# Kernel optimization log

Measured on AMD Instinct MI355X. Metric: run time of the kernel, lower is better.

## Reference

```python
import jax, jax.numpy as jnp
import numpy as np

A = -0.75  # torch bicubic coefficient
K = 5
K2 = K * K
IN_CH = 32 * 2 + 169 + 16 * 2 + 1  # 266
TIMESTEP = 0.5


def _cubic_w(t):
    # t in [0,1); weights for taps at offsets -1,0,1,2 (torch cubic convolution, A=-0.75)
    w1 = ((A + 2.0) * t - (A + 3.0)) * t * t + 1.0
    s = 1.0 - t
    w2 = ((A + 2.0) * s - (A + 3.0)) * s * s + 1.0
    u = t + 1.0
    w0 = ((A * u - 5.0 * A) * u + 8.0 * A) * u - 4.0 * A
    v = 2.0 - t
    w3 = ((A * v - 5.0 * A) * v + 8.0 * A) * v - 4.0 * A
    return (w0, w1, w2, w3)


def _conv3(x, w, b):
    y = jax.lax.conv_general_dilated(x, w, (1, 1), 'SAME',
                                     dimension_numbers=('NCHW', 'OIHW', 'NCHW'))
    return y + b[None, :, None, None]


def _lrelu(x):
    return jnp.where(x >= 0, x, 0.1 * x)


def _kernel_pred(x, w1, b1, w2, b2, w3, b3, ow, ob, ww, wb):
    f = _lrelu(_conv3(x, w1, b1))
    f = _lrelu(_conv3(f, w2, b2))
    f = _lrelu(_conv3(f, w3, b3))
    offsets = _conv3(f, ow, ob)                      # (B, 2*K2, H, W)
    weights = jax.nn.softmax(_conv3(f, ww, wb), axis=1)  # (B, K2, H, W)
    return offsets, weights


def _adacof_sample(image, offsets, weights):
    # bicubic grid_sample(padding_mode='border', align_corners=True) + weighted combine
    b, c, h, w = image.shape
    k2 = weights.shape[1]
    gx = jnp.arange(w, dtype=image.dtype)
    gy = jnp.arange(h, dtype=image.dtype)
    dx = offsets[:, 0::2]                # (b,k2,h,w)
    dy = offsets[:, 1::2]
    # with align_corners=True, normalize->unnormalize is identity
    sx = gx[None, None, None, :] + dx
    sy = gy[None, None, :, None] + dy
    x0 = jnp.floor(sx); tx = sx - x0
    y0 = jnp.floor(sy); ty = sy - y0
    wx = _cubic_w(tx)
    wy = _cubic_w(ty)
    xi = [jnp.clip(x0 + (i - 1.0), 0, w - 1).astype(jnp.int32) for i in range(4)]
    yi = [jnp.clip(y0 + (i - 1.0), 0, h - 1).astype(jnp.int32) for i in range(4)]
    imgf = image.reshape(b, c, h * w)
    gather = jax.vmap(lambda im, idx: im[:, idx])   # (c,hw),(n,)->(c,n)
    acc = jnp.zeros((b, c, k2, h, w), image.dtype)
    for i in range(4):
        for j in range(4):
            idx = (yi[i] * w + xi[j]).reshape(b, -1)
            g = gather(imgf, idx).reshape(b, c, k2, h, w)
            acc = acc + g * (wy[i] * wx[j])[:, None]
    return jnp.einsum('bckhw,bkhw->bchw', acc, weights)


def setup_inputs() -> dict:
    key = jax.random.key(0)
    ks = iter(jax.random.split(key, 64))
    d = {}
    d['frame1'] = jax.random.normal(next(ks), (2, 3, 256, 256), jnp.float32)
    d['frame2'] = jax.random.normal(next(ks), (2, 3, 256, 256), jnp.float32)
    d['feat1'] = jax.random.normal(next(ks), (2, 32, 256, 256), jnp.float32)
    d['feat2'] = jax.random.normal(next(ks), (2, 32, 256, 256), jnp.float32)
    d['corr'] = jax.random.normal(next(ks), (2, 169, 256, 256), jnp.float32)

    def conv_w(o, i):
        return jax.random.normal(next(ks), (o, i, 3, 3), jnp.float32) * 0.05

    # full-res encoder
    d['fr_w1'] = conv_w(16, 3); d['fr_b1'] = jnp.zeros((16,), jnp.float32)
    d['fr_w2'] = conv_w(16, 16); d['fr_b2'] = jnp.zeros((16,), jnp.float32)
    # default grid offsets for offset_head bias (dx,dy interleaved)
    off_bias = []
    for i in range(K):
        for j in range(K):
            off_bias.extend([j - K // 2, i - K // 2])
    off_bias = jnp.asarray(off_bias, jnp.float32)
    for p in ('kp1', 'kp2'):
        d[p + '_w1'] = conv_w(256, IN_CH); d[p + '_b1'] = jnp.zeros((256,), jnp.float32)
        d[p + '_w2'] = conv_w(256, 256); d[p + '_b2'] = jnp.zeros((256,), jnp.float32)
        d[p + '_w3'] = conv_w(128, 256); d[p + '_b3'] = jnp.zeros((128,), jnp.float32)
        d[p + '_ow'] = jax.random.normal(next(ks), (2 * K2, 128, 3, 3), jnp.float32) * 0.01
        d[p + '_ob'] = off_bias
        d[p + '_ww'] = jax.random.normal(next(ks), (K2, 128, 3, 3), jnp.float32) * 0.01
        d[p + '_wb'] = jnp.full((K2,), 1.0 / K2, jnp.float32)
    d['bl_w1'] = conv_w(64, IN_CH); d['bl_b1'] = jnp.zeros((64,), jnp.float32)
    d['bl_w2'] = conv_w(1, 64); d['bl_b2'] = jnp.zeros((1,), jnp.float32)
    return d


def reference(frame1, frame2, feat1, feat2, corr,
              fr_w1, fr_b1, fr_w2, fr_b2,
              kp1_w1, kp1_b1, kp1_w2, kp1_b2, kp1_w3, kp1_b3, kp1_ow, kp1_ob, kp1_ww, kp1_wb,
              kp2_w1, kp2_b1, kp2_w2, kp2_b2, kp2_w3, kp2_b3, kp2_ow, kp2_ob, kp2_ww, kp2_wb,
              bl_w1, bl_b1, bl_w2, bl_b2):
    b, _, h, w = frame1.shape
    fr1 = _lrelu(_conv3(_lrelu(_conv3(frame1, fr_w1, fr_b1)), fr_w2, fr_b2))
    fr2 = _lrelu(_conv3(_lrelu(_conv3(frame2, fr_w1, fr_b1)), fr_w2, fr_b2))
    t_map = jnp.full((b, 1, h, w), TIMESTEP, frame1.dtype)
    combined = jnp.concatenate([feat1, feat2, corr, fr1, fr2, t_map], axis=1)
    offsets1, weights1 = _kernel_pred(combined, kp1_w1, kp1_b1, kp1_w2, kp1_b2,
                                      kp1_w3, kp1_b3, kp1_ow, kp1_ob, kp1_ww, kp1_wb)
    offsets2, weights2 = _kernel_pred(combined, kp2_w1, kp2_b1, kp2_w2, kp2_b2,
                                      kp2_w3, kp2_b3, kp2_ow, kp2_ob, kp2_ww, kp2_wb)
    sample1 = _adacof_sample(frame1, offsets1, weights1)
    sample2 = _adacof_sample(frame2, offsets2, weights2)
    blend = jax.nn.sigmoid(_conv3(_lrelu(_conv3(combined, bl_w1, bl_b1)), bl_w2, bl_b2))
    output = blend * sample1 + (1.0 - blend) * sample2
    return (output, blend, offsets1, offsets2, weights1, weights2)
```

## Files before the change

kernel.cpp:

```cpp
#include <hip/hip_runtime.h>
#include <cstdint>
#include <cstddef>

#define H 256
#define W 256
#define HW (H*W)
#define BATCH 2
#define CIN_TILE 4

typedef __bf16 bf16x8 __attribute__((ext_vector_type(8)));
typedef float f32x4 __attribute__((ext_vector_type(4)));
typedef __attribute__((address_space(1))) uint32_t gu32_t;
typedef __attribute__((address_space(3))) uint32_t lu32_t;

__device__ __forceinline__ void async16(const void* g, void* l) {
  __builtin_amdgcn_global_load_lds((const gu32_t*)g, (lu32_t*)l, 16, 0, 0);
}

__device__ __forceinline__ ushort f2bf(float f) {
  uint u = __float_as_uint(f);
  return (ushort)((u + 0x7FFFu + ((u >> 16) & 1u)) >> 16);
}
__device__ __forceinline__ float lrelu_f(float v) { return v >= 0.f ? v : 0.1f * v; }

template<int EPI>
__global__ __launch_bounds__(256) void convmm_k(
    const ushort* __restrict__ act, const ushort* __restrict__ wgt,
    const float* __restrict__ bias, ushort* __restrict__ dstb,
    float* __restrict__ dsto, float* __restrict__ dstw,
    const ushort* __restrict__ zpage, int Cin, int CoutS)
{
  __shared__ __align__(16) ushort s_w[2304 * 8];
  __shared__ __align__(16) ushort s_b[1536 * 8];

  const int tid = threadIdx.x;
  const int sp = blockIdx.x;
  const int bx = (sp & 7) * 32, by = (sp >> 3) * 8;
  const int co0 = blockIdx.y * 64;
  const int wv = tid >> 6, lane = tid & 63;
  const int c = lane & 15, kq = lane >> 4;
  const int oy = wv * 2;

  int wsrc[9];
#pragma unroll
  for (int it = 0; it < 9; ++it) {
    int i = tid + it * 256;
    int co = i & 63, tk = i >> 6, tap = tk >> 2, kg = tk & 3;
    wsrc[it] = ((co0 + co) * 9 + tap) * Cin + kg * 8;
  }
  int bsrc[6];
#pragma unroll
  for (int it = 0; it < 6; ++it) {
    int i = tid + it * 256;
    int kg = i / 384, px = i - kg * 384;
    int row = px / 34, xx = px - row * 34;
    int gy = by + row - 1, gx = bx + xx - 1;
    bool ok = (px < 340) && ((unsigned)gy < (unsigned)H) && ((unsigned)gx < (unsigned)W);
    bsrc[it] = ok ? ((gy * W + gx) * Cin + kg * 8) : -1;
  }

  f32x4 acc[4][4];
#pragma unroll
  for (int a = 0; a < 4; ++a)
#pragma unroll
    for (int b2 = 0; b2 < 4; ++b2) acc[a][b2] = (f32x4){0.f, 0.f, 0.f, 0.f};

  const int nch = Cin >> 5;
  for (int ch = 0; ch < nch; ++ch) {
    const int c0 = ch << 5;
    __syncthreads();
#pragma unroll
    for (int it = 0; it < 9; ++it)
      async16(wgt + wsrc[it] + c0, &s_w[(size_t)(tid + it * 256) * 8]);
#pragma unroll
    for (int it = 0; it < 6; ++it) {
      const ushort* g = (bsrc[it] < 0) ? zpage : (act + bsrc[it] + c0);
      async16(g, &s_b[(size_t)(tid + it * 256) * 8]);
    }
    __syncthreads();

#pragma unroll
    for (int t = 0; t < 9; ++t) {
      const int dy = t / 3 - 1, dx = t % 3 - 1;
      bf16x8 B[4];
#pragma unroll
      for (int pf = 0; pf < 4; ++pf) {
        int p = (oy + (pf >> 1) + dy + 1) * 34 + (pf & 1) * 16 + dx + 1 + c;
        B[pf] = *(const bf16x8*)&s_b[(size_t)(kq * 384 + p) * 8];
      }
#pragma unroll
      for (int cf = 0; cf < 4; ++cf) {
        bf16x8 A = *(const bf16x8*)&s_w[(size_t)((t * 4 + kq) * 64 + cf * 16 + c) * 8];
#pragma unroll
        for (int pf = 0; pf < 4; ++pf)
          acc[cf][pf] = __builtin_amdgcn_mfma_f32_16x16x32_bf16(A, B[pf], acc[cf][pf], 0, 0, 0);
      }
    }
  }

  const int r4 = kq * 4;
#pragma unroll
  for (int cf = 0; cf < 4; ++cf) {
    int cob = co0 + cf * 16 + r4;
#pragma unroll
    for (int pf = 0; pf < 4; ++pf) {
      int gx2 = bx + (pf & 1) * 16 + c;
      int gy2 = by + oy + (pf >> 1);
      int gpix = gy2 * W + gx2;
      f32x4 v = acc[cf][pf];
      const float4 bv = *(const float4*)&bias[cob];
      if constexpr (EPI == 0) {
        ushort4 ov;
        float f0 = lrelu_f(v[0] + bv.x);
        float f1 = lrelu_f(v[1] + bv.y);
        float f2 = lrelu_f(v[2] + bv.z);
        float f3 = lrelu_f(v[3] + bv.w);
        ov.x = f2bf(f0); ov.y = f2bf(f1); ov.z = f2bf(f2); ov.w = f2bf(f3);
        *(ushort4*)&dstb[(size_t)gpix * CoutS + cob] = ov;
      } else {
        const float* bvp = &bv.x;
#pragma unroll
        for (int r = 0; r < 4; ++r) {
          int coa = cob + r;
          if (coa < 75) {
            float f = v[r] + bvp[r];
            if (coa < 50) dsto[(size_t)coa * HW + gpix] = f;
            else          dstw[(size_t)(coa - 50) * HW + gpix] = f;
          }
        }
      }
    }
  }
}

template<int CIN>
__global__ __launch_bounds__(256) void conv_fr_k(
    const float* __restrict__ sA, const float* __restrict__ sB, int mode,
    const float* __restrict__ wgt, const float* __restrict__ bias,
    float* __restrict__ dst)
{
  const int z = blockIdx.y;
  const float* src = (mode == 0)
      ? (((z >> 1) ? sB : sA) + (size_t)(z & 1) * 3 * HW)
      : (sA + (size_t)z * 16 * HW);
  float* out = dst + (size_t)z * 16 * HW;

  const int sp = blockIdx.x;
  const int bx = (sp & 7) * 32, by = (sp >> 3) * 32;
  const int tid = threadIdx.x;
  const int tx = tid & 15, ty = tid >> 4;

  __shared__ float s_in[CIN_TILE][34][36];
  float acc[16][2][2];
#pragma unroll
  for (int co = 0; co < 16; ++co) {
    acc[co][0][0] = 0.f; acc[co][0][1] = 0.f;
    acc[co][1][0] = 0.f; acc[co][1][1] = 0.f;
  }

  for (int c0 = 0; c0 < CIN; c0 += CIN_TILE) {
    __syncthreads();
    const int nst = CIN_TILE * 34 * 34;
    for (int i = tid; i < nst; i += 256) {
      int ci = i / (34 * 34);
      int r = i - ci * (34 * 34);
      int yy = r / 34;
      int xx = r - yy * 34;
      int gy = by + yy - 1, gx = bx + xx - 1;
      int cc = c0 + ci;
      float v = 0.f;
      if (cc < CIN && (unsigned)gy < (unsigned)H && (unsigned)gx < (unsigned)W)
        v = src[(size_t)cc * HW + gy * W + gx];
      s_in[ci][yy][xx] = v;
    }
    __syncthreads();

    const int cmax = (CIN - c0 < CIN_TILE) ? (CIN - c0) : CIN_TILE;
    for (int ci = 0; ci < cmax; ++ci) {
      float win[4][4];
#pragma unroll
      for (int iy = 0; iy < 4; ++iy)
#pragma unroll
        for (int ix = 0; ix < 4; ++ix)
          win[iy][ix] = s_in[ci][2 * ty + iy][2 * tx + ix];
#pragma unroll
      for (int co = 0; co < 16; ++co) {
        const float* wp = wgt + ((size_t)co * CIN + (c0 + ci)) * 9;
        float w0 = wp[0], w1 = wp[1], w2 = wp[2];
        float w3 = wp[3], w4 = wp[4], w5 = wp[5];
        float w6 = wp[6], w7 = wp[7], w8 = wp[8];
#pragma unroll
        for (int py = 0; py < 2; ++py)
#pragma unroll
          for (int px = 0; px < 2; ++px) {
            float s = acc[co][py][px];
            s += w0 * win[py + 0][px + 0];
            s += w1 * win[py + 0][px + 1];
            s += w2 * win[py + 0][px + 2];
            s += w3 * win[py + 1][px + 0];
            s += w4 * win[py + 1][px + 1];
            s += w5 * win[py + 1][px + 2];
            s += w6 * win[py + 2][px + 0];
            s += w7 * win[py + 2][px + 1];
            s += w8 * win[py + 2][px + 2];
            acc[co][py][px] = s;
          }
      }
    }
  }
#pragma unroll
  for (int co = 0; co < 16; ++co) {
    float bv = bias[co];
#pragma unroll
    for (int py = 0; py < 2; ++py)
#pragma unroll
      for (int px = 0; px < 2; ++px)
        out[(size_t)co * HW + (size_t)(by + 2 * ty + py) * W + (bx + 2 * tx + px)] =
            lrelu_f(acc[co][py][px] + bv);
  }
}

__global__ __launch_bounds__(256) void pack_k(
    const float* __restrict__ feat1, const float* __restrict__ feat2,
    const float* __restrict__ corr, const float* __restrict__ fr,
    ushort* __restrict__ comb, int b)
{
  int gid = blockIdx.x * 256 + threadIdx.x;
  int chunk = gid / HW;
  int p = gid - chunk * HW;
  int c0 = chunk * 32;

  uint u[16];
#pragma unroll
  for (int j = 0; j < 32; j += 2) {
    float f[2];
#pragma unroll
    for (int q = 0; q < 2; ++q) {
      int cc = c0 + j + q;
      float v;
      if (cc < 32)       v = feat1[(size_t)(b * 32 + cc) * HW + p];
      else if (cc < 64)  v = feat2[(size_t)(b * 32 + cc - 32) * HW + p];
      else if (cc < 233) v = corr[(size_t)(b * 169 + cc - 64) * HW + p];
      else if (cc < 249) v = fr[(size_t)(b * 16 + (cc - 233)) * HW + p];
      else if (cc < 265) v = fr[(size_t)((2 + b) * 16 + (cc - 249)) * HW + p];
      else if (cc == 265) v = 0.5f;
      else               v = 0.f;
      f[q] = v;
    }
    u[j >> 1] = (uint)f2bf(f[0]) | ((uint)f2bf(f[1]) << 16);
  }
  uint4* dst = (uint4*)&comb[(size_t)p * 288 + c0];
#pragma unroll
  for (int q = 0; q < 4; ++q) {
    uint4 t;
    t.x = u[q * 4 + 0]; t.y = u[q * 4 + 1]; t.z = u[q * 4 + 2]; t.w = u[q * 4 + 3];
    dst[q] = t;
  }
}

__global__ __launch_bounds__(256) void prep_w_k(
    const float* __restrict__ src, ushort* __restrict__ dst, int O, int I, int Ipad)
{
  int idx = blockIdx.x * 256 + threadIdx.x;
  int tot = O * 9 * Ipad;
  if (idx >= tot) return;
  int i = idx % Ipad;
  int r = idx / Ipad;
  int tap = r % 9;
  int o = r / 9;
  float v = (i < I) ? src[((size_t)o * I + i) * 9 + tap] : 0.f;
  dst[idx] = f2bf(v);
}

__global__ __launch_bounds__(256) void zfill_k(ushort* __restrict__ dst, int n)
{
  int idx = blockIdx.x * 256 + threadIdx.x;
  if (idx < n) dst[idx] = 0;
}

__global__ __launch_bounds__(128) void hbias_k(
    const float* __restrict__ ob, const float* __restrict__ wb, float* __restrict__ out)
{
  int i = threadIdx.x;
  float v = 0.f;
  if (i < 50) v = ob[i];
  else if (i < 75) v = wb[i - 50];
  out[i] = v;
}

__global__ __launch_bounds__(256) void blend2_k(
    const ushort* __restrict__ actD, const float* __restrict__ wgt,
    const float* __restrict__ b2, float* __restrict__ outp)
{
  int p = blockIdx.x * 256 + threadIdx.x;
  int y = p >> 8, x = p & 255;
  float acc = b2[0];
  for (int dy = -1; dy <= 1; ++dy) {
    int gy = y + dy;
    if ((unsigned)gy >= (unsigned)H) continue;
    for (int dx = -1; dx <= 1; ++dx) {
      int gx = x + dx;
      if ((unsigned)gx >= (unsigned)W) continue;
      int tap = (dy + 1) * 3 + (dx + 1);
      const ushort* rowp = actD + (size_t)(gy * W + gx) * 64;
#pragma unroll
      for (int c8 = 0; c8 < 8; ++c8) {
        uint4 v = *(const uint4*)&rowp[c8 * 8];
        const uint* vv = &v.x;
#pragma unroll
        for (int q = 0; q < 4; ++q) {
          float f0 = __uint_as_float(vv[q] << 16);
          float f1 = __uint_as_float(vv[q] & 0xFFFF0000u);
          int ci = c8 * 8 + q * 2;
          acc += f0 * wgt[ci * 9 + tap];
          acc += f1 * wgt[(ci + 1) * 9 + tap];
        }
      }
    }
  }
  outp[p] = 1.f / (1.f + expf(-acc));
}

__global__ __launch_bounds__(256) void softmax25_k(float* __restrict__ wr)
{
  int p = blockIdx.x * 256 + threadIdx.x;
  if (p >= HW) return;
  float v[25];
  float m = -1e30f;
#pragma unroll
  for (int k = 0; k < 25; ++k) {
    v[k] = wr[(size_t)k * HW + p];
    m = fmaxf(m, v[k]);
  }
  float s = 0.f;
#pragma unroll
  for (int k = 0; k < 25; ++k) {
    v[k] = expf(v[k] - m);
    s += v[k];
  }
  float inv = 1.f / s;
#pragma unroll
  for (int k = 0; k < 25; ++k)
    wr[(size_t)k * HW + p] = v[k] * inv;
}

__device__ __forceinline__ void cubic4(float t, float* cw)
{
  const float A_ = -0.75f;
  float t2 = t * t;
  cw[1] = ((A_ + 2.f) * t - (A_ + 3.f)) * t2 + 1.f;
  float s = 1.f - t;
  cw[2] = ((A_ + 2.f) * s - (A_ + 3.f)) * (s * s) + 1.f;
  float u = t + 1.f;
  cw[0] = ((A_ * u - 5.f * A_) * u + 8.f * A_) * u - 4.f * A_;
  float v = 2.f - t;
  cw[3] = ((A_ * v - 5.f * A_) * v + 8.f * A_) * v - 4.f * A_;
}

__global__ __launch_bounds__(256) void adacof_final_k(
    const float* __restrict__ frame1, const float* __restrict__ frame2,
    const float* __restrict__ off1, const float* __restrict__ off2,
    const float* __restrict__ wt1, const float* __restrict__ wt2,
    const float* __restrict__ blend, float* __restrict__ outp)
{
  int idx = blockIdx.x * 256 + threadIdx.x;
  if (idx >= BATCH * HW) return;
  int b = idx / HW, p = idx - b * HW;
  int y = p / W, x = p - y * W;

  float acc1[3] = {0.f, 0.f, 0.f};
  float acc2[3] = {0.f, 0.f, 0.f};

  auto samp = [&](const float* __restrict__ img, const float* __restrict__ off,
                  const float* __restrict__ wts, float* acc) {
    for (int k = 0; k < 25; ++k) {
      float dx = off[((size_t)b * 50 + 2 * k) * HW + p];
      float dy = off[((size_t)b * 50 + 2 * k + 1) * HW + p];
      float wk = wts[((size_t)b * 25 + k) * HW + p];
      float sx = (float)x + dx, sy = (float)y + dy;
      float x0 = floorf(sx), y0 = floorf(sy);
      float tx = sx - x0, ty = sy - y0;
      float wx[4], wy[4];
      cubic4(tx, wx);
      cubic4(ty, wy);
      int xi[4], yi[4];
#pragma unroll
      for (int i = 0; i < 4; ++i) {
        xi[i] = (int)fminf(fmaxf(x0 + (float)(i - 1), 0.f), (float)(W - 1));
        yi[i] = (int)fminf(fmaxf(y0 + (float)(i - 1), 0.f), (float)(H - 1));
      }
      const float* c0 = img + ((size_t)b * 3 + 0) * HW;
      const float* c1 = img + ((size_t)b * 3 + 1) * HW;
      const float* c2 = img + ((size_t)b * 3 + 2) * HW;
#pragma unroll
      for (int i = 0; i < 4; ++i) {
#pragma unroll
        for (int j = 0; j < 4; ++j) {
          float wf = wy[i] * wx[j] * wk;
          int q = yi[i] * W + xi[j];
          acc[0] += c0[q] * wf;
          acc[1] += c1[q] * wf;
          acc[2] += c2[q] * wf;
        }
      }
    }
  };

  samp(frame1, off1, wt1, acc1);
  samp(frame2, off2, wt2, acc2);

  float bl = blend[(size_t)b * HW + p];
#pragma unroll
  for (int ci = 0; ci < 3; ++ci)
    outp[((size_t)b * 3 + ci) * HW + p] = bl * acc1[ci] + (1.f - bl) * acc2[ci];
}

extern "C" void kernel_launch(void* const* d_in, const int* in_sizes, int n_in,
                              void* d_out, int out_size, void* d_ws, size_t ws_size,
                              hipStream_t stream)
{
  const float* frame1 = (const float*)d_in[0];
  const float* frame2 = (const float*)d_in[1];
  const float* feat1  = (const float*)d_in[2];
  const float* feat2  = (const float*)d_in[3];
  const float* corr   = (const float*)d_in[4];
  const float* fr_w1  = (const float*)d_in[5];
  const float* fr_b1  = (const float*)d_in[6];
  const float* fr_w2  = (const float*)d_in[7];
  const float* fr_b2  = (const float*)d_in[8];

  const float* kw1[2] = {(const float*)d_in[9],  (const float*)d_in[19]};
  const float* kb1[2] = {(const float*)d_in[10], (const float*)d_in[20]};
  const float* kw2[2] = {(const float*)d_in[11], (const float*)d_in[21]};
  const float* kb2[2] = {(const float*)d_in[12], (const float*)d_in[22]};
  const float* kw3[2] = {(const float*)d_in[13], (const float*)d_in[23]};
  const float* kb3[2] = {(const float*)d_in[14], (const float*)d_in[24]};
  const float* kow[2] = {(const float*)d_in[15], (const float*)d_in[25]};
  const float* kob[2] = {(const float*)d_in[16], (const float*)d_in[26]};
  const float* kww[2] = {(const float*)d_in[17], (const float*)d_in[27]};
  const float* kwb[2] = {(const float*)d_in[18], (const float*)d_in[28]};

  const float* bl_w1 = (const float*)d_in[29];
  const float* bl_b1 = (const float*)d_in[30];
  const float* bl_w2 = (const float*)d_in[31];
  const float* bl_b2 = (const float*)d_in[32];

  float* out = (float*)d_out;
  float* o_out   = out;
  float* o_blend = o_out   + (size_t)BATCH * 3 * HW;
  float* o_off1  = o_blend + (size_t)BATCH * 1 * HW;
  float* o_off2  = o_off1  + (size_t)BATCH * 50 * HW;
  float* o_w1    = o_off2  + (size_t)BATCH * 50 * HW;
  float* o_w2    = o_w1    + (size_t)BATCH * 25 * HW;

  size_t off = 0;
  char* wsb = (char*)d_ws;
  auto alloc = [&](size_t bytes) -> void* {
    void* pp = wsb + off;
    off += (bytes + 255) & ~(size_t)255;
    return pp;
  };
  ushort* zpage   = (ushort*)alloc(512);
  ushort* wp1[2]  = {(ushort*)alloc((size_t)256 * 9 * 288 * 2), (ushort*)alloc((size_t)256 * 9 * 288 * 2)};
  ushort* wp2[2]  = {(ushort*)alloc((size_t)256 * 9 * 256 * 2), (ushort*)alloc((size_t)256 * 9 * 256 * 2)};
  ushort* wp3[2]  = {(ushort*)alloc((size_t)128 * 9 * 256 * 2), (ushort*)alloc((size_t)128 * 9 * 256 * 2)};
  ushort* wph[2]  = {(ushort*)alloc((size_t)128 * 9 * 128 * 2), (ushort*)alloc((size_t)128 * 9 * 128 * 2)};
  ushort* wpb     = (ushort*)alloc((size_t)64 * 9 * 288 * 2);
  float*  hbias[2] = {(float*)alloc(128 * 4), (float*)alloc(128 * 4)};
  float*  tmp4    = (float*)alloc((size_t)4 * 16 * HW * 4);
  float*  frbuf   = (float*)alloc((size_t)4 * 16 * HW * 4);
  ushort* comb    = (ushort*)alloc((size_t)HW * 288 * 2);
  ushort* actA    = (ushort*)alloc((size_t)HW * 256 * 2);
  ushort* actB    = (ushort*)alloc((size_t)HW * 256 * 2);
  ushort* actC    = actA;
  ushort* actD    = actB;

  dim3 blk(256);

  hipMemsetAsync(zpage, 0, 512, stream);
  for (int p = 0; p < 2; ++p) {
    prep_w_k<<<dim3((256 * 9 * 288 + 255) / 256), blk, 0, stream>>>(kw1[p], wp1[p], 256, 266, 288);
    prep_w_k<<<dim3((256 * 9 * 256 + 255) / 256), blk, 0, stream>>>(kw2[p], wp2[p], 256, 256, 256);
    prep_w_k<<<dim3((128 * 9 * 256 + 255) / 256), blk, 0, stream>>>(kw3[p], wp3[p], 128, 256, 256);
    prep_w_k<<<dim3((50 * 9 * 128 + 255) / 256), blk, 0, stream>>>(kow[p], wph[p], 50, 128, 128);
    prep_w_k<<<dim3((25 * 9 * 128 + 255) / 256), blk, 0, stream>>>(kww[p], wph[p] + (size_t)50 * 9 * 128, 25, 128, 128);
    zfill_k<<<dim3((53 * 9 * 128 + 255) / 256), blk, 0, stream>>>(wph[p] + (size_t)75 * 9 * 128, 53 * 9 * 128);
    hbias_k<<<dim3(1), dim3(128), 0, stream>>>(kob[p], kwb[p], hbias[p]);
  }
  prep_w_k<<<dim3((64 * 9 * 288 + 255) / 256), blk, 0, stream>>>(bl_w1, wpb, 64, 266, 288);

  conv_fr_k<3><<<dim3(64, 4), blk, 0, stream>>>(frame1, frame2, 0, fr_w1, fr_b1, tmp4);
  conv_fr_k<16><<<dim3(64, 4), blk, 0, stream>>>(tmp4, nullptr, 1, fr_w2, fr_b2, frbuf);

  for (int b = 0; b < BATCH; ++b) {
    pack_k<<<dim3(9 * HW / 256), blk, 0, stream>>>(feat1, feat2, corr, frbuf, comb, b);

    for (int p = 0; p < 2; ++p) {
      float* ooff = (p ? o_off2 : o_off1) + (size_t)b * 50 * HW;
      float* oww  = (p ? o_w2   : o_w1)   + (size_t)b * 25 * HW;

      convmm_k<0><<<dim3(256, 4), blk, 0, stream>>>(comb, wp1[p], kb1[p], actA,
                                                    nullptr, nullptr, zpage, 288, 256);
      convmm_k<0><<<dim3(256, 4), blk, 0, stream>>>(actA, wp2[p], kb2[p], actB,
                                                    nullptr, nullptr, zpage, 256, 256);
      convmm_k<0><<<dim3(256, 2), blk, 0, stream>>>(actB, wp3[p], kb3[p], actC,
                                                    nullptr, nullptr, zpage, 256, 128);
      convmm_k<1><<<dim3(256, 2), blk, 0, stream>>>(actC, wph[p], hbias[p], nullptr,
                                                    ooff, oww, zpage, 128, 0);
      softmax25_k<<<dim3(HW / 256), blk, 0, stream>>>(oww);
    }

    convmm_k<0><<<dim3(256, 1), blk, 0, stream>>>(comb, wpb, bl_b1, actD,
                                                  nullptr, nullptr, zpage, 288, 64);
    blend2_k<<<dim3(HW / 256), blk, 0, stream>>>(actD, bl_w2, bl_b2, o_blend + (size_t)b * HW);
  }

  adacof_final_k<<<dim3((BATCH * HW + 255) / 256), blk, 0, stream>>>(
      frame1, frame2, o_off1, o_off2, o_w1, o_w2, o_blend, o_out);
}
```

Measured before the change: 1.484 ms.

## Batch both kernel-predictor branches via grid z, merge prep launches, split adacof taps

The two kernel-prediction conv chains now run as a single launch per layer using blockIdx.z with per-branch strides, when the workspace is large enough. Softmax for both branches is merged into one launch, and the weight and bias prep kernels are collapsed into single segmented launches. The adacof sampling kernel now spreads the 25 taps across 4 waves and reduces the partial sums through shared memory to raise parallelism. The cost is doubled activation buffers and an extra LDS reduction and barrier.

```diff
diff --git a/kernel.cpp b/kernel.cpp
--- a/kernel.cpp
+++ b/kernel.cpp
@@ -28,8 +28,16 @@
     const ushort* __restrict__ act, const ushort* __restrict__ wgt,
     const float* __restrict__ bias, ushort* __restrict__ dstb,
     float* __restrict__ dsto, float* __restrict__ dstw,
-    const ushort* __restrict__ zpage, int Cin, int CoutS)
-{
+    const ushort* __restrict__ zpage, int Cin, int CoutS,
+    int astride, int wstride, int bstride, int dstride)
+{
+  const int z = blockIdx.z;
+  act += (size_t)z * astride;
+  wgt += (size_t)z * wstride;
+  bias += (size_t)z * bstride;
+  if constexpr (EPI == 0) dstb += (size_t)z * dstride;
+  else { dsto += (size_t)z * (BATCH * 50 * HW); dstw += (size_t)z * (BATCH * 25 * HW); }
+
   __shared__ __align__(16) ushort s_w[2304 * 8];
   __shared__ __align__(16) ushort s_b[1536 * 8];
 
@@ -258,34 +266,43 @@
   }
 }
 
-__global__ __launch_bounds__(256) void prep_w_k(
-    const float* __restrict__ src, ushort* __restrict__ dst, int O, int I, int Ipad)
-{
-  int idx = blockIdx.x * 256 + threadIdx.x;
-  int tot = O * 9 * Ipad;
-  if (idx >= tot) return;
-  int i = idx % Ipad;
-  int r = idx / Ipad;
+struct PrepSeg { const float* src; ushort* dst; int O, I, Ipad; };
+struct PrepArgs { PrepSeg s[13]; int pre[14]; };
+
+__global__ __launch_bounds__(256) void prep_all_k(PrepArgs a)
+{
+  int gid = blockIdx.x * 256 + threadIdx.x;
+  if (gid >= a.pre[13]) return;
+  int si = 0;
+  while (gid >= a.pre[si + 1]) ++si;
+  int idx = gid - a.pre[si];
+  const PrepSeg sg = a.s[si];
+  int i = idx % sg.Ipad;
+  int r = idx / sg.Ipad;
   int tap = r % 9;
   int o = r / 9;
-  float v = (i < I) ? src[((size_t)o * I + i) * 9 + tap] : 0.f;
-  dst[idx] = f2bf(v);
-}
-
-__global__ __launch_bounds__(256) void zfill_k(ushort* __restrict__ dst, int n)
-{
-  int idx = blockIdx.x * 256 + threadIdx.x;
-  if (idx < n) dst[idx] = 0;
-}
-
-__global__ __launch_bounds__(128) void hbias_k(
-    const float* __restrict__ ob, const float* __restrict__ wb, float* __restrict__ out)
-{
+  float v = (i < sg.I) ? sg.src[((size_t)o * sg.I + i) * 9 + tap] : 0.f;
+  sg.dst[idx] = f2bf(v);
+}
+
+__global__ __launch_bounds__(256) void bias_all_k(
+    const float* kb1_0, const float* kb1_1, const float* kb2_0, const float* kb2_1,
+    const float* kb3_0, const float* kb3_1,
+    const float* ob0, const float* wb0, const float* ob1, const float* wb1,
+    float* bb1, float* bb2, float* bb3, float* bbh)
+{
+  int yq = blockIdx.y;
   int i = threadIdx.x;
-  float v = 0.f;
-  if (i < 50) v = ob[i];
-  else if (i < 75) v = wb[i - 50];
-  out[i] = v;
+  switch (yq) {
+    case 0: bb1[i] = kb1_0[i]; break;
+    case 1: bb1[256 + i] = kb1_1[i]; break;
+    case 2: bb2[i] = kb2_0[i]; break;
+    case 3: bb2[256 + i] = kb2_1[i]; break;
+    case 4: if (i < 128) bb3[i] = kb3_0[i]; break;
+    case 5: if (i < 128) bb3[128 + i] = kb3_1[i]; break;
+    case 6: if (i < 128) bbh[i]       = (i < 50) ? ob0[i] : ((i < 75) ? wb0[i - 50] : 0.f); break;
+    case 7: if (i < 128) bbh[128 + i] = (i < 50) ? ob1[i] : ((i < 75) ? wb1[i - 50] : 0.f); break;
+  }
 }
 
 __global__ __launch_bounds__(256) void blend2_k(
@@ -321,8 +338,10 @@
   outp[p] = 1.f / (1.f + expf(-acc));
 }
 
-__global__ __launch_bounds__(256) void softmax25_k(float* __restrict__ wr)
-{
+__global__ __launch_bounds__(256) void softmax25_k(float* __restrict__ w1,
+                                                   float* __restrict__ w2)
+{
+  float* wr = blockIdx.y ? w2 : w1;
   int p = blockIdx.x * 256 + threadIdx.x;
   if (p >= HW) return;
   float v[25];
@@ -363,17 +382,18 @@
     const float* __restrict__ wt1, const float* __restrict__ wt2,
     const float* __restrict__ blend, float* __restrict__ outp)
 {
-  int idx = blockIdx.x * 256 + threadIdx.x;
-  if (idx >= BATCH * HW) return;
-  int b = idx / HW, p = idx - b * HW;
-  int y = p / W, x = p - y * W;
-
-  float acc1[3] = {0.f, 0.f, 0.f};
-  float acc2[3] = {0.f, 0.f, 0.f};
+  __shared__ float s_red[4][64][6];
+  const int wv = threadIdx.x >> 6, lane = threadIdx.x & 63;
+  const int idx = blockIdx.x * 64 + lane;
+  const int b = idx / HW, p = idx - b * HW;
+  const int y = p >> 8, x = p & 255;
+
+  float a1[3] = {0.f, 0.f, 0.f};
+  float a2[3] = {0.f, 0.f, 0.f};
 
   auto samp = [&](const float* __restrict__ img, const float* __restrict__ off,
                   const float* __restrict__ wts, float* acc) {
-    for (int k = 0; k < 25; ++k) {
+    for (int k = wv; k < 25; k += 4) {
       float dx = off[((size_t)b * 50 + 2 * k) * HW + p];
       float dy = off[((size_t)b * 50 + 2 * k + 1) * HW + p];
       float wk = wts[((size_t)b * 25 + k) * HW + p];
@@ -406,13 +426,26 @@
     }
   };
 
-  samp(frame1, off1, wt1, acc1);
-  samp(frame2, off2, wt2, acc2);
-
-  float bl = blend[(size_t)b * HW + p];
-#pragma unroll
-  for (int ci = 0; ci < 3; ++ci)
-    outp[((size_t)b * 3 + ci) * HW + p] = bl * acc1[ci] + (1.f - bl) * acc2[ci];
+  samp(frame1, off1, wt1, a1);
+  samp(frame2, off2, wt2, a2);
+
+#pragma unroll
+  for (int c3 = 0; c3 < 3; ++c3) {
+    s_red[wv][lane][c3] = a1[c3];
+    s_red[wv][lane][3 + c3] = a2[c3];
+  }
+  __syncthreads();
+  if (wv == 0) {
+    float bl = blend[(size_t)b * HW + p];
+#pragma unroll
+    for (int c3 = 0; c3 < 3; ++c3) {
+      float r1 = s_red[0][lane][c3] + s_red[1][lane][c3] +
+                 s_red[2][lane][c3] + s_red[3][lane][c3];
+      float r2 = s_red[0][lane][3 + c3] + s_red[1][lane][3 + c3] +
+                 s_red[2][lane][3 + c3] + s_red[3][lane][3 + c3];
+      outp[((size_t)b * 3 + c3) * HW + p] = bl * r1 + (1.f - bl) * r2;
+    }
+  }
 }
 
 extern "C" void kernel_launch(void* const* d_in, const int* in_sizes, int n_in,
@@ -460,61 +493,97 @@
     off += (bytes + 255) & ~(size_t)255;
     return pp;
   };
-  ushort* zpage   = (ushort*)alloc(512);
-  ushort* wp1[2]  = {(ushort*)alloc((size_t)256 * 9 * 288 * 2), (ushort*)alloc((size_t)256 * 9 * 288 * 2)};
-  ushort* wp2[2]  = {(ushort*)alloc((size_t)256 * 9 * 256 * 2), (ushort*)alloc((size_t)256 * 9 * 256 * 2)};
-  ushort* wp3[2]  = {(ushort*)alloc((size_t)128 * 9 * 256 * 2), (ushort*)alloc((size_t)128 * 9 * 256 * 2)};
-  ushort* wph[2]  = {(ushort*)alloc((size_t)128 * 9 * 128 * 2), (ushort*)alloc((size_t)128 * 9 * 128 * 2)};
-  ushort* wpb     = (ushort*)alloc((size_t)64 * 9 * 288 * 2);
-  float*  hbias[2] = {(float*)alloc(128 * 4), (float*)alloc(128 * 4)};
-  float*  tmp4    = (float*)alloc((size_t)4 * 16 * HW * 4);
-  float*  frbuf   = (float*)alloc((size_t)4 * 16 * HW * 4);
-  ushort* comb    = (ushort*)alloc((size_t)HW * 288 * 2);
-  ushort* actA    = (ushort*)alloc((size_t)HW * 256 * 2);
-  ushort* actB    = (ushort*)alloc((size_t)HW * 256 * 2);
-  ushort* actC    = actA;
-  ushort* actD    = actB;
+  const size_t NEED_MERGED = 212700000;
+  const bool merged = ws_size >= NEED_MERGED;
+  const int NZ = merged ? 2 : 1;
+
+  ushort* zpage = (ushort*)alloc(512);
+  ushort* wp1   = (ushort*)alloc((size_t)2 * 256 * 9 * 288 * 2);
+  ushort* wp2   = (ushort*)alloc((size_t)2 * 256 * 9 * 256 * 2);
+  ushort* wp3   = (ushort*)alloc((size_t)2 * 128 * 9 * 256 * 2);
+  ushort* wph   = (ushort*)alloc((size_t)2 * 128 * 9 * 128 * 2);
+  ushort* wpb   = (ushort*)alloc((size_t)64 * 9 * 288 * 2);
+  float*  bb1   = (float*)alloc(2 * 256 * 4);
+  float*  bb2   = (float*)alloc(2 * 256 * 4);
+  float*  bb3   = (float*)alloc(2 * 128 * 4);
+  float*  bbh   = (float*)alloc(2 * 128 * 4);
+  float*  tmp4  = (float*)alloc((size_t)4 * 16 * HW * 4);
+  float*  frbuf = (float*)alloc((size_t)4 * 16 * HW * 4);
+  ushort* comb  = (ushort*)alloc((size_t)HW * 288 * 2);
+  ushort* actA  = (ushort*)alloc((size_t)NZ * HW * 256 * 2);
+  ushort* actB  = (ushort*)alloc((size_t)NZ * HW * 256 * 2);
 
   dim3 blk(256);
 
   hipMemsetAsync(zpage, 0, 512, stream);
-  for (int p = 0; p < 2; ++p) {
-    prep_w_k<<<dim3((256 * 9 * 288 + 255) / 256), blk, 0, stream>>>(kw1[p], wp1[p], 256, 266, 288);
-    prep_w_k<<<dim3((256 * 9 * 256 + 255) / 256), blk, 0, stream>>>(kw2[p], wp2[p], 256, 256, 256);
-    prep_w_k<<<dim3((128 * 9 * 256 + 255) / 256), blk, 0, stream>>>(kw3[p], wp3[p], 128, 256, 256);
-    prep_w_k<<<dim3((50 * 9 * 128 + 255) / 256), blk, 0, stream>>>(kow[p], wph[p], 50, 128, 128);
-    prep_w_k<<<dim3((25 * 9 * 128 + 255) / 256), blk, 0, stream>>>(kww[p], wph[p] + (size_t)50 * 9 * 128, 25, 128, 128);
-    zfill_k<<<dim3((53 * 9 * 128 + 255) / 256), blk, 0, stream>>>(wph[p] + (size_t)75 * 9 * 128, 53 * 9 * 128);
-    hbias_k<<<dim3(1), dim3(128), 0, stream>>>(kob[p], kwb[p], hbias[p]);
-  }
-  prep_w_k<<<dim3((64 * 9 * 288 + 255) / 256), blk, 0, stream>>>(bl_w1, wpb, 64, 266, 288);
+  {
+    PrepArgs pa;
+    const int W1 = 256 * 9 * 288, W2 = 256 * 9 * 256, W3 = 128 * 9 * 256;
+    const int OW = 50 * 9 * 128, WW = 25 * 9 * 128, ZW = 53 * 9 * 128;
+    const int WB = 64 * 9 * 288;
+    const int HP = 128 * 9 * 128;
+    PrepSeg segs[13] = {
+      {kw1[0], wp1,                    256, 266, 288},
+      {kw1[1], wp1 + W1,               256, 266, 288},
+      {kw2[0], wp2,                    256, 256, 256},
+      {kw2[1], wp2 + W2,               256, 256, 256},
+      {kw3[0], wp3,                    128, 256, 256},
+      {kw3[1], wp3 + W3,               128, 256, 256},
+      {kow[0], wph,                     50, 128, 128},
+      {kww[0], wph + OW,                25, 128, 128},
+      {nullptr, wph + OW + WW,          53,   0, 128},
+      {kow[1], wph + HP,                50, 128, 128},
+      {kww[1], wph + HP + OW,           25, 128, 128},
+      {nullptr, wph + HP + OW + WW,     53,   0, 128},
+      {bl_w1,  wpb,                     64, 266, 288},
+    };
+    int tots[13] = {W1, W1, W2, W2, W3, W3, OW, WW, ZW, OW, WW, ZW, WB};
+    pa.pre[0] = 0;
+    for (int s = 0; s < 13; ++s) { pa.s[s] = segs[s]; pa.pre[s + 1] = pa.pre[s] + tots[s]; }
+    int nblk = (pa.pre[13] + 255) / 256;
+    prep_all_k<<<dim3(nblk), blk, 0, stream>>>(pa);
+  }
+  bias_all_k<<<dim3(1, 8), blk, 0, stream>>>(kb1[0], kb1[1], kb2[0], kb2[1],
+                                             kb3[0], kb3[1], kob[0], kwb[0],
+                                             kob[1], kwb[1], bb1, bb2, bb3, bbh);
 
   conv_fr_k<3><<<dim3(64, 4), blk, 0, stream>>>(frame1, frame2, 0, fr_w1, fr_b1, tmp4);
   conv_fr_k<16><<<dim3(64, 4), blk, 0, stream>>>(tmp4, nullptr, 1, fr_w2, fr_b2, frbuf);
 
+  const int W1 = 256 * 9 * 288, W2 = 256 * 9 * 256, W3 = 128 * 9 * 256;
+  const int HP = 128 * 9 * 128;
+
   for (int b = 0; b < BATCH; ++b) {
     pack_k<<<dim3(9 * HW / 256), blk, 0, stream>>>(feat1, feat2, corr, frbuf, comb, b);
 
-    for (int p = 0; p < 2; ++p) {
-      float* ooff = (p ? o_off2 : o_off1) + (size_t)b * 50 * HW;
-      float* oww  = (p ? o_w2   : o_w1)   + (size_t)b * 25 * HW;
-
-      convmm_k<0><<<dim3(256, 4), blk, 0, stream>>>(comb, wp1[p], kb1[p], actA,
-                                                    nullptr, nullptr, zpage, 288, 256);
-      convmm_k<0><<<dim3(256, 4), blk, 0, stream>>>(actA, wp2[p], kb2[p], actB,
-                                                    nullptr, nullptr, zpage, 256, 256);
-      convmm_k<0><<<dim3(256, 2), blk, 0, stream>>>(actB, wp3[p], kb3[p], actC,
-                                                    nullptr, nullptr, zpage, 256, 128);
-      convmm_k<1><<<dim3(256, 2), blk, 0, stream>>>(actC, wph[p], hbias[p], nullptr,
-                                                    ooff, oww, zpage, 128, 0);
-      softmax25_k<<<dim3(HW / 256), blk, 0, stream>>>(oww);
-    }
-
-    convmm_k<0><<<dim3(256, 1), blk, 0, stream>>>(comb, wpb, bl_b1, actD,
-                                                  nullptr, nullptr, zpage, 288, 64);
-    blend2_k<<<dim3(HW / 256), blk, 0, stream>>>(actD, bl_w2, bl_b2, o_blend + (size_t)b * HW);
-  }
-
-  adacof_final_k<<<dim3((BATCH * HW + 255) / 256), blk, 0, stream>>>(
+    for (int pp = 0; pp < 2 / NZ; ++pp) {
+      const size_t po = pp;
+      convmm_k<0><<<dim3(256, 4, NZ), blk, 0, stream>>>(
+          comb, wp1 + po * W1, bb1 + po * 256, actA + po * (size_t)HW * 256,
+          nullptr, nullptr, zpage, 288, 256, 0, W1, 256, HW * 256);
+      convmm_k<0><<<dim3(256, 4, NZ), blk, 0, stream>>>(
+          actA + po * (size_t)HW * 256, wp2 + po * W2, bb2 + po * 256,
+          actB + po * (size_t)HW * 256,
+          nullptr, nullptr, zpage, 256, 256, HW * 256, W2, 256, HW * 256);
+      convmm_k<0><<<dim3(256, 2, NZ), blk, 0, stream>>>(
+          actB + po * (size_t)HW * 256, wp3 + po * W3, bb3 + po * 128,
+          actA + po * (size_t)HW * 128,
+          nullptr, nullptr, zpage, 256, 128, HW * 256, W3, 128, HW * 128);
+      convmm_k<1><<<dim3(256, 2, NZ), blk, 0, stream>>>(
+          actA + po * (size_t)HW * 128, wph + po * HP, bbh + po * 128, nullptr,
+          o_off1 + (size_t)b * 50 * HW + po * (size_t)BATCH * 50 * HW,
+          o_w1 + (size_t)b * 25 * HW + po * (size_t)BATCH * 25 * HW,
+          zpage, 128, 0, HW * 128, HP, 128, 0);
+    }
+    softmax25_k<<<dim3(HW / 256, 2), blk, 0, stream>>>(
+        o_w1 + (size_t)b * 25 * HW, o_w2 + (size_t)b * 25 * HW);
+
+    convmm_k<0><<<dim3(256, 1, 1), blk, 0, stream>>>(
+        comb, wpb, bl_b1, actB, nullptr, nullptr, zpage, 288, 64, 0, 0, 0, 0);
+    blend2_k<<<dim3(HW / 256), blk, 0, stream>>>(actB, bl_w2, bl_b2,
+                                                 o_blend + (size_t)b * HW);
+  }
+
+  adacof_final_k<<<dim3(BATCH * HW / 64), blk, 0, stream>>>(
       frame1, frame2, o_off1, o_off2, o_w1, o_w2, o_blend, o_out);
 }
```

Measured after the change: 1.485 ms. Within noise of the previous version (+0.1%).
